# Kernel tuning notes

Hardware: AMD Instinct MI355X
Metric: run time of the kernel (lower is better)

The kernel has to match this reference:

```python
import jax, jax.numpy as jnp
import numpy as np
import math

NN_K = 32          # num_neighbor = ceil(k/dilation) = 32
MAP_SIZE = 32
GROUP = 4


def _fibonacci_sphere(samples):
    # matches fibonacci_sphere(samples, randomize=False): rnd = 1.0
    pts = [[0.0, 0.0, 0.0]]
    offset = 2.0 / samples
    increment = math.pi * (3.0 - math.sqrt(5.0))
    for i in range(samples - 1):
        y = i * offset - 1 + offset / 2.0
        r = math.sqrt(1.0 - y * y)
        phi = ((i + 1.0) % samples) * increment
        pts.append([math.cos(phi) * r, y, math.sin(phi) * r])
    return np.asarray(pts, dtype=np.float32)


def setup_inputs() -> dict:
    B, N, C_in, C_out = 8, 2048, 64, 128
    key = jax.random.key(0)
    ks = jax.random.split(key, 6)
    x = jax.random.normal(ks[0], (B, 3, N), dtype=jnp.float32)
    feature = jax.random.normal(ks[1], (B, C_in, N), dtype=jnp.float32)
    neigh_indexs = jax.random.randint(ks[2], (B, N, NN_K), 0, N, dtype=jnp.int32)
    B_rff = jax.random.normal(ks[3], (7, MAP_SIZE), dtype=jnp.float32)  # frozen RFF proj
    kernels = jnp.asarray(_fibonacci_sphere(NN_K).T)                    # [3, NN_K], frozen
    mlp_w = jax.random.normal(ks[4], (C_in, 2 * MAP_SIZE), dtype=jnp.float32) * 0.05
    mlp_b = jnp.zeros((C_in,), dtype=jnp.float32)
    conv_w = jax.random.normal(ks[5], (C_out, 2 * C_in * NN_K), dtype=jnp.float32) * 0.02
    conv_b = jnp.zeros((C_out,), dtype=jnp.float32)
    return {"x": x, "feature": feature, "neigh_indexs": neigh_indexs,
            "B_rff": B_rff, "kernels": kernels,
            "mlp_w": mlp_w, "mlp_b": mlp_b, "conv_w": conv_w, "conv_b": conv_b}


def _topkmax(perm):
    # two normalization passes over axis=1 (rows), squaring in between, then hard threshold
    perm = perm / (jnp.sum(perm, axis=1, keepdims=True) + 1e-6)
    perm = perm * perm
    perm = perm / (jnp.sum(perm, axis=1, keepdims=True) + 1e-6)
    return jnp.where(perm > 0.1, perm, 0.0)


def _paiconv(x, feature, neigh_indexs, B_rff, kernels, mlp_w, mlp_b, conv_w, conv_b):
    bsz, C, N = feature.shape           # B, num_feat, num_pts
    nn_k = neigh_indexs.shape[-1]
    xp = jnp.transpose(x, (0, 2, 1))    # [B, N, 3]

    # neighbor gather of coordinates -> [B*N, nn, 3]
    x_neighs = jax.vmap(lambda p, i: p[i])(xp, neigh_indexs).reshape(bsz * N, nn_k, 3)
    x_rep = jnp.broadcast_to(x_neighs[:, :1, :], x_neighs.shape)
    x_rel = x_neighs - x_rep
    x_dis = jnp.linalg.norm(x_rel, axis=-1, keepdims=True)

    # random Fourier features + 1x1 conv (mlp)
    pos = (2.0 * math.pi) * jnp.concatenate([x_rep, x_rel, x_dis], axis=-1)  # [BN, nn, 7]
    xf = pos @ B_rff                                                          # [BN, nn, 32]
    xf = jnp.concatenate([jnp.sin(xf), jnp.cos(xf)], axis=-1)                 # [BN, nn, 64]
    xf = jnp.einsum('oc,bnc->bon', mlp_w, xf) + mlp_b[None, :, None]          # [BN, C, nn]

    # neighbor gather of features -> [BN, C, nn], concat with positional feats
    fp = jnp.transpose(feature, (0, 2, 1))                                    # [B, N, C]
    f_nb = jax.vmap(lambda p, i: p[i])(fp, neigh_indexs).reshape(bsz * N, nn_k, C)
    feats = jnp.concatenate([jnp.transpose(f_nb, (0, 2, 1)), xf], axis=1)     # [BN, 2C, nn]

    # permutation/attention matrix
    one_pad = jnp.zeros((nn_k, nn_k), dtype=x.dtype).at[0, 0].set(1.0)
    perm = x_rel @ kernels + one_pad                                          # [BN, nn, nn]
    perm = jnp.where(perm > 0, perm, 0.0)
    perm = _topkmax(perm)

    if C > 3:  # static channel shuffle with group=4
        feats = feats.reshape(bsz * N, GROUP, 2 * C // GROUP, nn_k)
        feats = jnp.transpose(feats, (0, 2, 1, 3)).reshape(bsz * N, 2 * C, nn_k)

    feats = feats @ perm                                                      # [BN, 2C, nn]
    feats = feats.reshape(bsz * N, 2 * C * nn_k)
    out = feats @ conv_w.T + conv_b                                           # [BN, out_c]
    return jnp.transpose(out.reshape(bsz, N, -1), (0, 2, 1))                  # [B, out_c, N]


def reference(x, feature, neigh_indexs, B_rff, kernels, mlp_w, mlp_b, conv_w, conv_b):
    return _paiconv(x, feature, neigh_indexs, B_rff, kernels, mlp_w, mlp_b, conv_w, conv_b)
```

## Files before the change

### kernel.cpp

```cpp
#include <hip/hip_runtime.h>
#include <hip/hip_bf16.h>

typedef unsigned short ushort_t;
typedef __attribute__((ext_vector_type(8))) short short8;
typedef __attribute__((ext_vector_type(4))) float floatx4;

#define TWO_PI 6.28318530717958647692f

__device__ __forceinline__ float bf2f(ushort_t u) {
  union { unsigned u; float f; } v; v.u = ((unsigned)u) << 16; return v.f;
}
__device__ __forceinline__ unsigned pk(float a, float b) {
  union { __hip_bfloat162 h2; unsigned u; } v;
  v.h2 = __float22bfloat162_rn(make_float2(a, b));
  return v.u;
}
__device__ __forceinline__ float ldin(const void* p, int idx, bool bf) {
  return bf ? bf2f(((const ushort_t*)p)[idx]) : ((const float*)p)[idx];
}
__device__ __forceinline__ bool detect_bf16(const void* xv) {
  const ushort_t* us = (const ushort_t*)xv;
  unsigned u = us[threadIdx.x & 63];
  int e = (u >> 7) & 0xFF;
  bool good = (e >= 110) && (e <= 133);
  unsigned long long m = __ballot(good);
  return __builtin_popcountll(m) >= 52;
}
__device__ __forceinline__ uint4 pack8f(const float* p) {
  float4 a = *(const float4*)p, b = *(const float4*)(p + 4);
  uint4 r;
  r.x = pk(a.x, a.y); r.y = pk(a.z, a.w);
  r.z = pk(b.x, b.y); r.w = pk(b.z, b.w);
  return r;
}

__device__ __forceinline__ void gload16(const void* g, void* l) {
  __builtin_amdgcn_global_load_lds(
      (const __attribute__((address_space(1))) unsigned*)g,
      (__attribute__((address_space(3))) unsigned*)l, 16, 0, 0);
}

__global__ __launch_bounds__(256) void paiconv_prep(
    const void* __restrict__ xprobe, const void* __restrict__ feat,
    ushort_t* __restrict__ Ft, const void* __restrict__ W,
    ushort_t* __restrict__ Wc)
{
  const bool bfm = detect_bf16(xprobe);
  const int t = threadIdx.x;
  __shared__ ushort_t tile[64 * 72];

  if (blockIdx.x >= 256) {
    int i = ((blockIdx.x - 256) * 256 + t) << 3;
    int n = i >> 12, rem = i & 4095;
    int c = rem >> 5, j = rem & 31;
    int src = (n << 12) + (((c & 31) * 4 + (c >> 5)) << 5) + j;
    if (bfm) *(uint4*)(Wc + i) = *(const uint4*)((const ushort_t*)W + src);
    else     *(uint4*)(Wc + i) = pack8f((const float*)W + src);
    return;
  }

  const int bb = blockIdx.x >> 5;
  const int n0 = (blockIdx.x & 31) << 6;
  {
    const int c = t & 63, ng = t >> 6;
    size_t base = (((size_t)(bb * 64 + c)) << 11) + n0 + (ng << 4);
    ushort_t v[16];
    if (bfm) {
      const ushort_t* fp_ = (const ushort_t*)feat + base;
      uint4 a = *(const uint4*)fp_, b2 = *(const uint4*)(fp_ + 8);
      unsigned uu[8] = {a.x, a.y, a.z, a.w, b2.x, b2.y, b2.z, b2.w};
#pragma unroll
      for (int e = 0; e < 8; ++e) {
        v[2 * e] = (ushort_t)(uu[e] & 0xffff);
        v[2 * e + 1] = (ushort_t)(uu[e] >> 16);
      }
    } else {
      const float* fp_ = (const float*)feat + base;
#pragma unroll
      for (int k = 0; k < 16; k += 2) {
        unsigned u = pk(fp_[k], fp_[k + 1]);
        v[k] = (ushort_t)(u & 0xffff);
        v[k + 1] = (ushort_t)(u >> 16);
      }
    }
#pragma unroll
    for (int k = 0; k < 16; ++k) tile[(ng * 16 + k) * 72 + c] = v[k];
  }
  __syncthreads();
  {
    const int nn = t >> 2, qtr = t & 3;
    uint4 w0 = *(const uint4*)(tile + nn * 72 + qtr * 16);
    uint4 w1 = *(const uint4*)(tile + nn * 72 + qtr * 16 + 8);
    ushort_t* dst = Ft + (((size_t)(bb * 2048 + n0 + nn)) << 6) + (qtr << 4);
    *(uint4*)dst = w0;
    *(uint4*)(dst + 8) = w1;
  }
}

#define SFPT 5184
__global__ __launch_bounds__(256) void paiconv_phase1(
    const void* __restrict__ x,
    const ushort_t* __restrict__ Ft,
    const int*  __restrict__ nbr,
    const void* __restrict__ Brff,
    const void* __restrict__ kern,
    const void* __restrict__ mlpw,
    const void* __restrict__ mlpb,
    ushort_t*   __restrict__ Ag)
{
  const bool bfm = detect_bf16(x);
  const int t = threadIdx.x;
  const int p0 = blockIdx.x << 1;
  const int b  = p0 >> 11;
  const int w = t >> 6, lane = t & 63, lrow = lane & 15, quad = lane >> 4;

  __shared__ ushort_t sRt[64 * 72];
  __shared__ ushort_t sF[SFPT];
  __shared__ ushort_t sP[2 * 32 * 40];
  __shared__ float sRel[2][32][3];
  __shared__ float sDis[2][32];
  __shared__ float sRep[2][3];
  __shared__ float sBr[224];

  const int gpt = t >> 7, gj = (t >> 2) & 31, gch = t & 3;
  const int gidx = nbr[((p0 + gpt) << 5) + gj];
  const ushort_t* gfr = Ft + (((size_t)(b * 2048 + gidx)) << 6) + (gch << 4);
  uint4 g0 = ((const uint4*)gfr)[0];
  uint4 g1 = ((const uint4*)gfr)[1];

  const int pj = t & 31;
  const float kn0 = ldin(kern, pj, bfm);
  const float kn1 = ldin(kern, 32 + pj, bfm);
  const float kn2 = ldin(kern, 64 + pj, bfm);
  const int mc = (w << 4) + lrow;
  const float bv = ldin(mlpb, mc, bfm);

  short8 mb0, mb1;
  if (bfm) {
    const ushort_t* mp = (const ushort_t*)mlpw + mc * 64;
    mb0 = *(const short8*)(mp + (quad << 3));
    mb1 = *(const short8*)(mp + 32 + (quad << 3));
  } else {
    const float* mp = (const float*)mlpw + mc * 64;
    uint4 u0 = pack8f(mp + (quad << 3));
    uint4 u1 = pack8f(mp + 32 + (quad << 3));
    mb0 = *(short8*)&u0;
    mb1 = *(short8*)&u1;
  }

  if (t < 224) sBr[t] = ldin(Brff, t, bfm);
  if (t < 64) {
    int pt = t >> 5, i = t & 31;
    int p = p0 + pt;
    int idx  = nbr[(p << 5) + i];
    int idx0 = nbr[(p << 5)];
    int xo = b * 6144;
    float rx = ldin(x, xo + idx0, bfm);
    float ry = ldin(x, xo + 2048 + idx0, bfm);
    float rz = ldin(x, xo + 4096 + idx0, bfm);
    float cx = ldin(x, xo + idx, bfm);
    float cy = ldin(x, xo + 2048 + idx, bfm);
    float cz = ldin(x, xo + 4096 + idx, bfm);
    float dx = cx - rx, dy = cy - ry, dz = cz - rz;
    sRel[pt][i][0] = dx; sRel[pt][i][1] = dy; sRel[pt][i][2] = dz;
    sDis[pt][i] = sqrtf(dx * dx + dy * dy + dz * dz);
    if (i == 0) { sRep[pt][0] = rx; sRep[pt][1] = ry; sRep[pt][2] = rz; }
  }
  __syncthreads();

  {
    int jn = t >> 2, mh = (t & 3) << 3;
    int pt = jn >> 5, j = jn & 31;
    float pos[7];
    pos[0] = TWO_PI * sRep[pt][0]; pos[1] = TWO_PI * sRep[pt][1];
    pos[2] = TWO_PI * sRep[pt][2];
    pos[3] = TWO_PI * sRel[pt][j][0]; pos[4] = TWO_PI * sRel[pt][j][1];
    pos[5] = TWO_PI * sRel[pt][j][2];
    pos[6] = TWO_PI * sDis[pt][j];
    unsigned sw[4], cw[4];
#pragma unroll
    for (int mm = 0; mm < 8; mm += 2) {
      float a0 = 0.f, a1 = 0.f;
#pragma unroll
      for (int d = 0; d < 7; ++d) {
        a0 += pos[d] * sBr[d * 32 + mh + mm];
        a1 += pos[d] * sBr[d * 32 + mh + mm + 1];
      }
      sw[mm >> 1] = pk(__sinf(a0), __sinf(a1));
      cw[mm >> 1] = pk(__cosf(a0), __cosf(a1));
    }
    ushort_t* rb = sRt + jn * 72;
    *(uint4*)(rb + mh)      = make_uint4(sw[0], sw[1], sw[2], sw[3]);
    *(uint4*)(rb + 32 + mh) = make_uint4(cw[0], cw[1], cw[2], cw[3]);
  }
  if (t < 128) {
    int pt = t >> 6, h = (t >> 5) & 1;
    float col[16];
    float s1 = 0.f;
#pragma unroll
    for (int il = 0; il < 16; ++il) {
      int i = h * 16 + il;
      float v = sRel[pt][i][0] * kn0 + sRel[pt][i][1] * kn1 + sRel[pt][i][2] * kn2;
      if (i == 0 && pj == 0) v += 1.0f;
      v = fmaxf(v, 0.f);
      col[il] = v; s1 += v;
    }
    s1 += __shfl_xor(s1, 32, 64);
    float inv1 = 1.0f / (s1 + 1e-6f);
    float s2 = 0.f;
#pragma unroll
    for (int il = 0; il < 16; ++il) { float v = col[il] * inv1; v = v * v; col[il] = v; s2 += v; }
    s2 += __shfl_xor(s2, 32, 64);
    float inv2 = 1.0f / (s2 + 1e-6f);
    unsigned pw[8];
#pragma unroll
    for (int il = 0; il < 16; il += 2) {
      float v0 = col[il] * inv2;     v0 = (v0 > 0.1f) ? v0 : 0.f;
      float v1 = col[il + 1] * inv2; v1 = (v1 > 0.1f) ? v1 : 0.f;
      pw[il >> 1] = pk(v0, v1);
    }
    ushort_t* dst = sP + pt * 1280 + pj * 40 + h * 16;
    *(uint4*)dst       = make_uint4(pw[0], pw[1], pw[2], pw[3]);
    *(uint4*)(dst + 8) = make_uint4(pw[4], pw[5], pw[6], pw[7]);
  }
  __syncthreads();

  const int rbase = (64 + mc) * 40 + ((4 + w) << 3);

#pragma unroll
  for (int pt = 0; pt < 2; ++pt) {
    {
#pragma unroll
      for (int half = 0; half < 2; ++half) {
        int mt = pt * 2 + half;
        const ushort_t* rp = sRt + (mt * 16 + lrow) * 72 + (quad << 3);
        short8 a0 = *(const short8*)rp;
        short8 a1 = *(const short8*)(rp + 32);
        floatx4 acc = {0.f, 0.f, 0.f, 0.f};
        acc = __builtin_amdgcn_mfma_f32_16x16x32_bf16(a0, mb0, acc, 0, 0, 0);
        acc = __builtin_amdgcn_mfma_f32_16x16x32_bf16(a1, mb1, acc, 0, 0, 0);
        int j0 = (half << 4) + (quad << 2);
        *(uint2*)(sF + rbase + j0) =
            make_uint2(pk(acc[0] + bv, acc[1] + bv), pk(acc[2] + bv, acc[3] + bv));
      }
      if (gpt == pt) {
        ushort_t* fp_ = sF + gch * 648 + gj;
        unsigned uu[8] = {g0.x, g0.y, g0.z, g0.w, g1.x, g1.y, g1.z, g1.w};
#pragma unroll
        for (int u = 0; u < 8; ++u) {
          fp_[(2 * u) * 40]     = (ushort_t)(uu[u] & 0xffff);
          fp_[(2 * u + 1) * 40] = (ushort_t)(uu[u] >> 16);
        }
      }
    }
    __syncthreads();

    {
      const ushort_t* Pp = sP + pt * 1280;
      short8 a0 = *(const short8*)(Pp + lrow * 40 + (quad << 3));
      short8 a1 = *(const short8*)(Pp + (16 + lrow) * 40 + (quad << 3));
      size_t prow = ((size_t)(p0 + pt)) << 12;
#pragma unroll
      for (int nt = 0; nt < 2; ++nt) {
        int blk = w * 2 + nt;
        int cidx = (blk << 4) + lrow;
        short8 bfg = *(const short8*)(sF + cidx * 40 + (blk << 3) + (quad << 3));
        floatx4 z = {0.f, 0.f, 0.f, 0.f};
        floatx4 c0 = __builtin_amdgcn_mfma_f32_16x16x32_bf16(a0, bfg, z, 0, 0, 0);
        floatx4 c1 = __builtin_amdgcn_mfma_f32_16x16x32_bf16(a1, bfg, z, 0, 0, 0);
        ushort_t* ad = Ag + prow + cidx * 32 + (quad << 2);
        *(uint2*)ad        = make_uint2(pk(c0[0], c0[1]), pk(c0[2], c0[3]));
        *(uint2*)(ad + 16) = make_uint2(pk(c1[0], c1[1]), pk(c1[2], c1[3]));
      }
    }
    if (pt == 0) __syncthreads();
  }
}

__global__ __launch_bounds__(512) void paiconv_gemm(
    const ushort_t* __restrict__ A,
    const ushort_t* __restrict__ Wc,
    float* __restrict__ part)
{
  __shared__ ushort_t lAs[2 * 64 * 64];
  __shared__ ushort_t lBs[2 * 128 * 64];
  const int m0 = blockIdx.x << 6;
  const int K0 = blockIdx.y << 11;
  const int t = threadIdx.x;
  const int w = t >> 6, lane = t & 63;
  const int wm = w & 1, wn = w >> 1, lrow = lane & 15, quad = lane >> 4;
  const int sx = lrow & 7;

  const int srow = t >> 3, schk = t & 7;
  const int gchk = schk ^ (srow & 7);
  const ushort_t* Agp  = A  + (size_t)(m0 + srow) * 4096 + K0 + (gchk << 3);
  const ushort_t* Bgp0 = Wc + (size_t)srow * 4096        + K0 + (gchk << 3);
  const ushort_t* Bgp1 = Wc + (size_t)(64 + srow) * 4096 + K0 + (gchk << 3);
  const int wb = w << 9;

  floatx4 acc[2][2];
#pragma unroll
  for (int i = 0; i < 2; ++i)
#pragma unroll
    for (int j = 0; j < 2; ++j) acc[i][j] = (floatx4){0.f, 0.f, 0.f, 0.f};

#define STAGE(buf, kbn) do { int off_ = (kbn) << 6;                         \
    gload16(Agp  + off_, lAs + ((buf) << 12) + wb);                         \
    gload16(Bgp0 + off_, lBs + ((buf) << 13) + wb);                         \
    gload16(Bgp1 + off_, lBs + ((buf) << 13) + 4096 + wb); } while (0)

  STAGE(0, 0);
  __syncthreads();

  int cur = 0;
  for (int kb = 0; kb < 32; ++kb) {
    if (kb + 1 < 32) STAGE(cur ^ 1, kb + 1);
    const ushort_t* la = lAs + (cur << 12);
    const ushort_t* lb = lBs + (cur << 13);
#pragma unroll
    for (int kk = 0; kk < 2; ++kk) {
      int ch = ((((kk << 2) + quad) ^ sx) << 3);
      short8 af0 = *(const short8*)(la + (((wm << 5) + lrow) << 6) + ch);
      short8 af1 = *(const short8*)(la + (((wm << 5) + 16 + lrow) << 6) + ch);
#pragma unroll
      for (int ni = 0; ni < 2; ++ni) {
        short8 bf = *(const short8*)(lb + (((wn << 5) + (ni << 4) + lrow) << 6) + ch);
        acc[0][ni] = __builtin_amdgcn_mfma_f32_16x16x32_bf16(af0, bf, acc[0][ni], 0, 0, 0);
        acc[1][ni] = __builtin_amdgcn_mfma_f32_16x16x32_bf16(af1, bf, acc[1][ni], 0, 0, 0);
      }
    }
    __syncthreads();
    cur ^= 1;
  }
#undef STAGE

  float* dst = part + ((size_t)blockIdx.y << 21);
#pragma unroll
  for (int mi = 0; mi < 2; ++mi)
#pragma unroll
    for (int ni = 0; ni < 2; ++ni)
#pragma unroll
      for (int r = 0; r < 4; ++r) {
        int m = m0 + (wm << 5) + (mi << 4) + (quad << 2) + r;
        int n = (wn << 5) + (ni << 4) + lrow;
        dst[(size_t)m * 128 + n] = acc[mi][ni][r];
      }
}

__global__ __launch_bounds__(256) void paiconv_reduce(
    const void* __restrict__ xprobe, const float* __restrict__ part,
    const void* __restrict__ bias, void* __restrict__ out)
{
  const bool bfm = detect_bf16(xprobe);
  __shared__ float buf[128 * 65];
  const int m0 = blockIdx.x << 6;
  const int b = m0 >> 11, n0 = m0 & 2047;
  const int t = threadIdx.x;

#pragma unroll
  for (int i = 0; i < 8; ++i) {
    int idx = (i * 256 + t) << 2;
    int mt = idx >> 7, c = idx & 127;
    size_t o = (size_t)(m0 + mt) * 128 + c;
    float4 v0 = *(const float4*)(part + o);
    float4 v1 = *(const float4*)(part + (1u << 21) + o);
    buf[(c + 0) * 65 + mt] = v0.x + v1.x + ldin(bias, c + 0, bfm);
    buf[(c + 1) * 65 + mt] = v0.y + v1.y + ldin(bias, c + 1, bfm);
    buf[(c + 2) * 65 + mt] = v0.z + v1.z + ldin(bias, c + 2, bfm);
    buf[(c + 3) * 65 + mt] = v0.w + v1.w + ldin(bias, c + 3, bfm);
  }
  __syncthreads();
#pragma unroll
  for (int i = 0; i < 8; ++i) {
    int idx = (i * 256 + t) << 2;
    int c = idx >> 6, nl = idx & 63;
    float v0 = buf[c * 65 + nl], v1 = buf[c * 65 + nl + 1];
    float v2 = buf[c * 65 + nl + 2], v3 = buf[c * 65 + nl + 3];
    size_t o = (size_t)b * 262144 + (size_t)c * 2048 + n0 + nl;
    if (bfm) *(uint2*)((ushort_t*)out + o) = make_uint2(pk(v0, v1), pk(v2, v3));
    else     *(float4*)((float*)out + o) = make_float4(v0, v1, v2, v3);
  }
}

extern "C" void kernel_launch(void* const* d_in, const int* in_sizes, int n_in,
                              void* d_out, int out_size, void* d_ws, size_t ws_size,
                              hipStream_t stream) {
  const void* x     = d_in[0];
  const void* feat  = d_in[1];
  const int*  nbr   = (const int*)d_in[2];
  const void* Brff  = d_in[3];
  const void* kern  = d_in[4];
  const void* mlpw  = d_in[5];
  const void* mlpb  = d_in[6];
  const void* convw = d_in[7];
  const void* convb = d_in[8];

  char* ws = (char*)d_ws;
  ushort_t* A   = (ushort_t*)ws;
  ushort_t* Wcv = (ushort_t*)(ws + (size_t)134217728);
  float*    prt = (float*)(ws + (size_t)135266304);
  ushort_t* Ft  = (ushort_t*)(ws + (size_t)152043520);

  paiconv_prep<<<512, 256, 0, stream>>>(x, feat, Ft, convw, Wcv);
  paiconv_phase1<<<8192, 256, 0, stream>>>(x, Ft, nbr, Brff, kern, mlpw, mlpb, A);
  paiconv_gemm<<<dim3(256, 2, 1), 512, 0, stream>>>(A, Wcv, prt);
  paiconv_reduce<<<256, 256, 0, stream>>>(x, prt, convb, d_out);
}
```

Baseline: 162.4 us.

## Triple-buffer GEMM LDS staging with explicit vmcnt waits and barriers

Moves the split-K GEMM main loop from a double buffer to a three-stage LDS ring. The loop is unrolled by three and uses explicit s_waitcnt vmcnt counts plus raw barriers, so two tiles of global-to-LDS loads stay in flight while the current tile is computed. This aims to hide global load latency behind the MFMA work. In exchange it uses 50% more shared memory, which may lower occupancy, and correctness now relies on the hand-counted vmcnt values matching the loads gload16 actually issues.

```diff
diff --git a/kernel.cpp b/kernel.cpp
--- a/kernel.cpp
+++ b/kernel.cpp
@@ -282,8 +282,8 @@
     const ushort_t* __restrict__ Wc,
     float* __restrict__ part)
 {
-  __shared__ ushort_t lAs[2 * 64 * 64];
-  __shared__ ushort_t lBs[2 * 128 * 64];
+  __shared__ ushort_t lAs[3 * 64 * 64];
+  __shared__ ushort_t lBs[3 * 128 * 64];
   const int m0 = blockIdx.x << 6;
   const int K0 = blockIdx.y << 11;
   const int t = threadIdx.x;
@@ -304,35 +304,47 @@
 #pragma unroll
     for (int j = 0; j < 2; ++j) acc[i][j] = (floatx4){0.f, 0.f, 0.f, 0.f};
 
-#define STAGE(buf, kbn) do { int off_ = (kbn) << 6;                         \
-    gload16(Agp  + off_, lAs + ((buf) << 12) + wb);                         \
-    gload16(Bgp0 + off_, lBs + ((buf) << 13) + wb);                         \
-    gload16(Bgp1 + off_, lBs + ((buf) << 13) + 4096 + wb); } while (0)
+#define STAGE(buf, kbn) do { int off_ = (kbn) << 6;                          \
+    gload16(Agp  + off_, lAs + (buf) * 4096 + wb);                           \
+    gload16(Bgp0 + off_, lBs + (buf) * 8192 + wb);                           \
+    gload16(Bgp1 + off_, lBs + (buf) * 8192 + 4096 + wb); } while (0)
+
+#define COMPUTE(buf) do {                                                    \
+    const ushort_t* la_ = lAs + (buf) * 4096;                                \
+    const ushort_t* lb_ = lBs + (buf) * 8192;                                \
+    _Pragma("unroll")                                                        \
+    for (int kk = 0; kk < 2; ++kk) {                                         \
+      int ch = ((((kk << 2) + quad) ^ sx) << 3);                             \
+      short8 af0 = *(const short8*)(la_ + (((wm << 5) + lrow) << 6) + ch);   \
+      short8 af1 = *(const short8*)(la_ + (((wm << 5) + 16 + lrow) << 6) + ch); \
+      _Pragma("unroll")                                                      \
+      for (int ni = 0; ni < 2; ++ni) {                                       \
+        short8 bf = *(const short8*)(lb_ + (((wn << 5) + (ni << 4) + lrow) << 6) + ch); \
+        acc[0][ni] = __builtin_amdgcn_mfma_f32_16x16x32_bf16(af0, bf, acc[0][ni], 0, 0, 0); \
+        acc[1][ni] = __builtin_amdgcn_mfma_f32_16x16x32_bf16(af1, bf, acc[1][ni], 0, 0, 0); \
+      } } } while (0)
+
+#define VMW(n) asm volatile("s_waitcnt vmcnt(" #n ")" ::: "memory")
+#define BAR() __builtin_amdgcn_s_barrier()
+#define SB0() __builtin_amdgcn_sched_barrier(0)
 
   STAGE(0, 0);
-  __syncthreads();
-
-  int cur = 0;
-  for (int kb = 0; kb < 32; ++kb) {
-    if (kb + 1 < 32) STAGE(cur ^ 1, kb + 1);
-    const ushort_t* la = lAs + (cur << 12);
-    const ushort_t* lb = lBs + (cur << 13);
-#pragma unroll
-    for (int kk = 0; kk < 2; ++kk) {
-      int ch = ((((kk << 2) + quad) ^ sx) << 3);
-      short8 af0 = *(const short8*)(la + (((wm << 5) + lrow) << 6) + ch);
-      short8 af1 = *(const short8*)(la + (((wm << 5) + 16 + lrow) << 6) + ch);
-#pragma unroll
-      for (int ni = 0; ni < 2; ++ni) {
-        short8 bf = *(const short8*)(lb + (((wn << 5) + (ni << 4) + lrow) << 6) + ch);
-        acc[0][ni] = __builtin_amdgcn_mfma_f32_16x16x32_bf16(af0, bf, acc[0][ni], 0, 0, 0);
-        acc[1][ni] = __builtin_amdgcn_mfma_f32_16x16x32_bf16(af1, bf, acc[1][ni], 0, 0, 0);
-      }
-    }
-    __syncthreads();
-    cur ^= 1;
-  }
+  STAGE(1, 1);
+
+  for (int g = 0; g < 10; ++g) {
+    const int kb = g * 3;
+    STAGE(2, kb + 2); VMW(6); BAR(); SB0(); COMPUTE(0); BAR();
+    STAGE(0, kb + 3); VMW(6); BAR(); SB0(); COMPUTE(1); BAR();
+    STAGE(1, kb + 4); VMW(6); BAR(); SB0(); COMPUTE(2); BAR();
+  }
+  VMW(3); BAR(); SB0(); COMPUTE(0);
+  VMW(0); BAR(); SB0(); COMPUTE(1);
+
 #undef STAGE
+#undef COMPUTE
+#undef VMW
+#undef BAR
+#undef SB0
 
   float* dst = part + ((size_t)blockIdx.y << 21);
 #pragma unroll
```

After: 162.3 us. About the same (-0.0%).
